# Kernel optimization log

Measured on AMD Instinct MI355X. Metric: run time of the kernel, lower is better.

## Reference

```python
import jax, jax.numpy as jnp
import numpy as np

B, Q, K, D = 16, 2048, 2048, 512


def setup_inputs() -> dict:
    key = jax.random.key(0)
    kq, kk, kv, kl = jax.random.split(key, 4)
    queries = jax.random.normal(kq, (B, Q, D), dtype=jnp.float32)
    keys = jax.random.normal(kk, (B, K, D), dtype=jnp.float32)
    values = jax.random.normal(kv, (B, K, D), dtype=jnp.float32)
    # lengths in [1, K] so no row is fully masked
    valid_lens = jax.random.randint(kl, (B,), 1, K + 1, dtype=jnp.int32)
    return {"queries": queries, "keys": keys, "values": values, "valid_lens": valid_lens}


def reference(queries, keys, values, valid_lens):
    # scores: [B, Q, K]
    scale = 1.0 / jnp.sqrt(jnp.asarray(queries.shape[-1], queries.dtype))
    scores = jnp.einsum('bqd,bkd->bqk', queries, keys) * scale
    # 1D valid_lens: per-batch key-length mask (positions >= len are masked)
    key_pos = jnp.arange(scores.shape[-1])  # [K]
    mask = key_pos[None, None, :] >= valid_lens[:, None, None]  # [B, 1->Q, K]
    scores = jnp.where(mask, -jnp.inf, scores)
    weights = jax.nn.softmax(scores, axis=-1)  # [B, Q, K]
    # dropout is identity in eval mode (deterministic reference)
    context = jnp.einsum('bqk,bkd->bqd', weights, values)  # [B, Q, D]
    return context, weights
```

## Files before the change

### kernel.cpp

```cpp
#include <hip/hip_runtime.h>
#include <stdint.h>

typedef __bf16 bf16_t;
typedef bf16_t bf16x8 __attribute__((ext_vector_type(8)));
typedef bf16_t bf16x4_t __attribute__((ext_vector_type(4)));
typedef float f32x4 __attribute__((ext_vector_type(4)));

#define NB 16
#define NQ 2048
#define NK 2048
#define ND 512
#define SCALE 0.04419417382415922f

typedef __attribute__((address_space(3))) uint32_t lds_u32;
typedef __attribute__((address_space(1))) const uint32_t glb_u32;

__device__ __forceinline__ float4 ld4(const float* p) { return *(const float4*)p; }

__device__ __forceinline__ f32x4 mfma16(bf16x8 a, bf16x8 b, f32x4 c) {
  return __builtin_amdgcn_mfma_f32_16x16x32_bf16(a, b, c, 0, 0, 0);
}

__global__ __launch_bounds__(256) void prep_kernel(const float* __restrict__ Qf,
                                                   const float* __restrict__ Kf,
                                                   const float* __restrict__ Vf,
                                                   bf16_t* __restrict__ Qb,
                                                   bf16_t* __restrict__ Kb,
                                                   bf16_t* __restrict__ VT,
                                                   const int* __restrict__ lens) {
  int x = blockIdx.x;
  int b = blockIdx.y;
  int z = blockIdx.z;
  int t = threadIdx.x;

  if (z == 2) {
    int kb = x >> 2, dq = (x & 3) * 128;
    if (kb * 32 >= lens[b]) return;
    const float* vsrc = Vf + ((size_t)b * NK + kb * 32) * ND;
    bf16_t* dst = VT + ((size_t)(b * 64 + kb)) * (512 * 32);
    __shared__ alignas(16) bf16_t Ls[32][128];
#pragma unroll
    for (int i = 0; i < 4; ++i) {
      int p = i * 256 + t;
      int k = p >> 5, c4 = p & 31;
      float4 v = ld4(vsrc + (size_t)k * ND + dq + c4 * 4);
      union { bf16_t h[4]; uint2 u; } pk;
      pk.h[0] = (bf16_t)v.x; pk.h[1] = (bf16_t)v.y;
      pk.h[2] = (bf16_t)v.z; pk.h[3] = (bf16_t)v.w;
      *(uint2*)(&Ls[k][c4 * 4]) = pk.u;
    }
    __syncthreads();
    int d = dq + (t >> 1);
    int h = t & 1;
    int sr = d >> 1;
#pragma unroll
    for (int gg = 0; gg < 2; ++gg) {
      int g = h * 2 + gg;
      bf16x8 v;
#pragma unroll
      for (int j = 0; j < 8; ++j) v[j] = Ls[g * 8 + j][d - dq];
      int slot = (((d & 1) << 2) | g) ^ (sr & 7);
      *(bf16x8*)(dst + ((size_t)sr * 8 + slot) * 8) = v;
    }
    return;
  }

  const float* src = z ? Kf : Qf;
  bf16_t* dst = z ? Kb : Qb;
  int rt = x >> 4, kt = x & 15;
  const float* s = src + ((size_t)b * 2048 + (size_t)rt * 128) * 512 + kt * 32;
  bf16_t* dtile = dst + (((size_t)b * 16 + rt) * 16 + kt) * 4096;
#pragma unroll
  for (int i = 0; i < 2; ++i) {
    int d = i * 256 + t;
    int r = d >> 2, slot = d & 3;
    int c = slot ^ ((r >> 1) & 3);
    const float* p = s + (size_t)r * 512 + c * 8;
    float4 v0 = ld4(p), v1 = ld4(p + 4);
    bf16x8 o;
    o[0] = (bf16_t)v0.x; o[1] = (bf16_t)v0.y; o[2] = (bf16_t)v0.z; o[3] = (bf16_t)v0.w;
    o[4] = (bf16_t)v1.x; o[5] = (bf16_t)v1.y; o[6] = (bf16_t)v1.z; o[7] = (bf16_t)v1.w;
    *(bf16x8*)(dtile + (size_t)d * 8) = o;
  }
}

__global__ __launch_bounds__(256, 3) void qk_kernel(const bf16_t* __restrict__ Qb,
                                                    const bf16_t* __restrict__ Kb,
                                                    float* __restrict__ P,
                                                    float* __restrict__ psum,
                                                    const int* __restrict__ lens) {
  int bid = blockIdx.x;
  int swz = (bid & 7) * 512 + (bid >> 3);
  int b = swz >> 8;
  int tile = swz & 255;
  int qt = tile >> 4, nt = tile & 15;

  int len = lens[b];
  int q0 = qt * 128;
  int col0 = nt * 128;
  if (col0 >= len) return;

  __shared__ alignas(16) bf16_t As[2][4096];
  __shared__ alignas(16) bf16_t Bs[2][4096];
  __shared__ float rsm[128];

  int t = threadIdx.x;
  int lane = t & 63;
  int wid = t >> 6;
  int wm = wid >> 1, wn = wid & 1;
  int l15 = lane & 15, l4 = lane >> 4;

  float* prow = P + ((size_t)b * NQ + q0) * NK;
  const bf16_t* qtile = Qb + (((size_t)b * 16 + qt) * 16) * 4096;
  const bf16_t* ktile = Kb + (((size_t)b * 16 + nt) * 16) * 4096;

  f32x4 acc[4][4];
  f32x4 zz = {0.f, 0.f, 0.f, 0.f};
#pragma unroll
  for (int mi = 0; mi < 4; ++mi)
#pragma unroll
    for (int ni = 0; ni < 4; ++ni) acc[mi][ni] = zz;

  int eo = wid * 512 + lane * 8;

  auto stage = [&](int kt2, int buf) {
    const bf16_t* qa = qtile + (size_t)kt2 * 4096;
    const bf16_t* ka = ktile + (size_t)kt2 * 4096;
    bf16_t* la = &As[buf][0];
    bf16_t* lb = &Bs[buf][0];
#pragma unroll
    for (int j = 0; j < 2; ++j) {
      __builtin_amdgcn_global_load_lds((glb_u32*)(qa + j * 2048 + eo),
                                       (lds_u32*)(la + j * 2048 + wid * 512), 16, 0, 0);
      __builtin_amdgcn_global_load_lds((glb_u32*)(ka + j * 2048 + eo),
                                       (lds_u32*)(lb + j * 2048 + wid * 512), 16, 0, 0);
    }
  };

  auto compute = [&](int buf) {
    bf16x8 af[4], bv[4];
#pragma unroll
    for (int mi = 0; mi < 4; ++mi) {
      int row = wm * 64 + mi * 16 + l15;
      int ch = row * 4 + (l4 ^ ((row >> 1) & 3));
      af[mi] = *(const bf16x8*)(&As[buf][ch * 8]);
    }
#pragma unroll
    for (int ni = 0; ni < 4; ++ni) {
      int row = wn * 64 + ni * 16 + l15;
      int ch = row * 4 + (l4 ^ ((row >> 1) & 3));
      bv[ni] = *(const bf16x8*)(&Bs[buf][ch * 8]);
    }
#pragma unroll
    for (int mi = 0; mi < 4; ++mi)
#pragma unroll
      for (int ni = 0; ni < 4; ++ni)
        acc[mi][ni] = mfma16(af[mi], bv[ni], acc[mi][ni]);
  };

  stage(0, 0);
  __syncthreads();
#pragma unroll 1
  for (int kt2 = 0; kt2 < 16; ++kt2) {
    if (kt2 + 1 < 16) stage(kt2 + 1, (kt2 + 1) & 1);
    compute(kt2 & 1);
    __syncthreads();
  }

  float rsum[4][4];
#pragma unroll
  for (int mi = 0; mi < 4; ++mi)
#pragma unroll
    for (int r = 0; r < 4; ++r) rsum[mi][r] = 0.f;

#pragma unroll
  for (int mi = 0; mi < 4; ++mi) {
#pragma unroll
    for (int ni = 0; ni < 4; ++ni) {
      int col = col0 + wn * 64 + ni * 16 + l15;
      bool valid = col < len;
#pragma unroll
      for (int r = 0; r < 4; ++r) {
        float e = valid ? __expf(acc[mi][ni][r] * SCALE) : 0.f;
        bf16_t eb = (bf16_t)e;
        rsum[mi][r] += (float)eb;
        bf16_t* purow =
            (bf16_t*)(prow + (size_t)(wm * 64 + mi * 16 + l4 * 4 + r) * NK) + 2048;
        purow[col] = eb;
      }
    }
  }

#pragma unroll
  for (int off = 1; off < 16; off <<= 1)
#pragma unroll
    for (int mi = 0; mi < 4; ++mi)
#pragma unroll
      for (int r = 0; r < 4; ++r)
        rsum[mi][r] += __shfl_xor(rsum[mi][r], off, 64);

  if (wn == 0 && l15 == 0) {
#pragma unroll
    for (int mi = 0; mi < 4; ++mi)
#pragma unroll
      for (int r = 0; r < 4; ++r)
        rsm[wm * 64 + mi * 16 + l4 * 4 + r] = rsum[mi][r];
  }
  __syncthreads();
  if (wn == 1 && l15 == 0) {
#pragma unroll
    for (int mi = 0; mi < 4; ++mi)
#pragma unroll
      for (int r = 0; r < 4; ++r) {
        int row = wm * 64 + mi * 16 + l4 * 4 + r;
        psum[((size_t)b * 16 + nt) * NQ + q0 + row] = rsum[mi][r] + rsm[row];
      }
  }
}

__global__ __launch_bounds__(512, 4) void pv_kernel(float* __restrict__ P,
                                                    const bf16_t* __restrict__ VT,
                                                    float* __restrict__ ctx,
                                                    const float* __restrict__ psum,
                                                    const int* __restrict__ lens) {
  int bid = blockIdx.x;
  int b = bid & 15, qt = bid >> 4;
  int q0 = qt * 64;
  int len = lens[b];
  int nsteps = (len + 31) >> 5;
  int nvalid = (len + 127) >> 7;

  __shared__ alignas(16) bf16_t Ps[2][64 * 32];
  __shared__ float rcp[64];

  int t = threadIdx.x;
  if (t < 64) {
    float s = 0.f;
    for (int i = 0; i < nvalid; ++i) s += psum[((size_t)b * 16 + i) * NQ + q0 + t];
    rcp[t] = 1.0f / s;
  }
  __syncthreads();

  float* prow = P + ((size_t)b * NQ + q0) * NK;
  const bf16_t* vtb = VT + ((size_t)b * 64) * (512 * 32);

  int lane = t & 63, wid = t >> 6;
  int l15 = lane & 15, l4 = lane >> 4;

  f32x4 acc[4][4];
  f32x4 zz = {0.f, 0.f, 0.f, 0.f};
#pragma unroll
  for (int mi = 0; mi < 4; ++mi)
#pragma unroll
    for (int ni = 0; ni < 4; ++ni) acc[mi][ni] = zz;

  int srow = t >> 3, sc4 = t & 7;
  float rr = rcp[srow];
  const bf16_t* purow = (const bf16_t*)(prow + (size_t)srow * NK) + 2048;

  int vchunk[4];
#pragma unroll
  for (int ni = 0; ni < 4; ++ni) {
    int d = wid * 64 + ni * 16 + l15;
    vchunk[ni] = ((d >> 1) * 8 + ((((d & 1) << 2) | l4) ^ ((d >> 1) & 7))) * 8;
  }

  bf16x4_t pld;

  auto stage_load = [&](int ks) {
    pld = *(const bf16x4_t*)(purow + ks * 32 + sc4 * 4);
  };
  auto stage_finish = [&](int ks, int buf) {
    float4 w;
    w.x = (float)pld[0] * rr; w.y = (float)pld[1] * rr;
    w.z = (float)pld[2] * rr; w.w = (float)pld[3] * rr;
    *(float4*)(prow + (size_t)srow * NK + ks * 32 + sc4 * 4) = w;
    int sr = srow >> 1;
    int slot = (((srow & 1) << 2) | (sc4 >> 1)) ^ (sr & 7);
    union { bf16_t h[4]; uint2 u; } pk;
    pk.h[0] = (bf16_t)w.x; pk.h[1] = (bf16_t)w.y;
    pk.h[2] = (bf16_t)w.z; pk.h[3] = (bf16_t)w.w;
    *(uint2*)(&Ps[buf][((size_t)sr * 8 + slot) * 8 + (sc4 & 1) * 4]) = pk.u;
  };
  auto compute = [&](int ks, int cur) {
    const bf16_t* vsrc = vtb + (size_t)ks * (512 * 32);
    bf16x8 bv[4];
#pragma unroll
    for (int ni = 0; ni < 4; ++ni)
      bv[ni] = *(const bf16x8*)(vsrc + vchunk[ni]);
    bf16x8 af[4];
#pragma unroll
    for (int mi = 0; mi < 4; ++mi) {
      int row = mi * 16 + l15;
      af[mi] = *(const bf16x8*)(&Ps[cur][((row >> 1) * 8 + ((((row & 1) << 2) | l4) ^ ((row >> 1) & 7))) * 8]);
    }
#pragma unroll
    for (int mi = 0; mi < 4; ++mi)
#pragma unroll
      for (int ni = 0; ni < 4; ++ni)
        acc[mi][ni] = mfma16(af[mi], bv[ni], acc[mi][ni]);
  };

  stage_load(0);
  stage_finish(0, 0);
  __syncthreads();
#pragma unroll 1
  for (int ks = 0; ks < nsteps; ++ks) {
    int cur = ks & 1;
    if (ks + 1 < nsteps) stage_load(ks + 1);
    compute(ks, cur);
    if (ks + 1 < nsteps) stage_finish(ks + 1, cur ^ 1);
    __syncthreads();
  }

  {
    float4 z = make_float4(0.f, 0.f, 0.f, 0.f);
    for (int c = nsteps * 32 + sc4 * 4; c < NK; c += 32)
      *(float4*)(prow + (size_t)srow * NK + c) = z;
  }

  float* crow = ctx + ((size_t)b * NQ + q0) * ND + wid * 64;
#pragma unroll
  for (int mi = 0; mi < 4; ++mi)
#pragma unroll
    for (int ni = 0; ni < 4; ++ni)
#pragma unroll
      for (int r = 0; r < 4; ++r)
        crow[(size_t)(mi * 16 + l4 * 4 + r) * ND + ni * 16 + l15] = acc[mi][ni][r];
}

extern "C" void kernel_launch(void* const* d_in, const int* in_sizes, int n_in,
                              void* d_out, int out_size, void* d_ws, size_t ws_size,
                              hipStream_t stream) {
  const float* Q = (const float*)d_in[0];
  const float* K = (const float*)d_in[1];
  const float* V = (const float*)d_in[2];
  const int* lens = (const int*)d_in[3];

  float* ctx = (float*)d_out;
  float* P = ctx + (size_t)NB * NQ * ND;

  float* psum = (float*)d_ws;
  char* base = (char*)d_ws + (size_t)NB * 16 * NQ * sizeof(float);
  bf16_t* Qb = (bf16_t*)base;
  bf16_t* Kb = (bf16_t*)(base + (size_t)NB * NQ * ND * 2);
  bf16_t* VT = (bf16_t*)(base + (size_t)2 * NB * NQ * ND * 2);

  prep_kernel<<<dim3(256, 16, 3), 256, 0, stream>>>(Q, K, V, Qb, Kb, VT, lens);
  qk_kernel<<<dim3(4096), 256, 0, stream>>>(Qb, Kb, P, psum, lens);
  pv_kernel<<<dim3(512), 512, 0, stream>>>(P, VT, ctx, psum, lens);
}
```

Before: 284.1 us.

## Enlarge QK tile to 256x256 with 8 waves and deeper k-step

```diff
diff --git a/kernel.cpp b/kernel.cpp
--- a/kernel.cpp
+++ b/kernel.cpp
@@ -84,97 +84,99 @@
   }
 }
 
-__global__ __launch_bounds__(256, 3) void qk_kernel(const bf16_t* __restrict__ Qb,
+__global__ __launch_bounds__(512, 2) void qk_kernel(const bf16_t* __restrict__ Qb,
                                                     const bf16_t* __restrict__ Kb,
                                                     float* __restrict__ P,
                                                     float* __restrict__ psum,
                                                     const int* __restrict__ lens) {
   int bid = blockIdx.x;
-  int swz = (bid & 7) * 512 + (bid >> 3);
-  int b = swz >> 8;
-  int tile = swz & 255;
-  int qt = tile >> 4, nt = tile & 15;
+  int swz = (bid & 7) * 128 + (bid >> 3);
+  int b = swz >> 6;
+  int rest = swz & 63;
+  int qt = rest >> 3, nt = rest & 7;
 
   int len = lens[b];
-  int q0 = qt * 128;
-  int col0 = nt * 128;
+  int q0 = qt * 256;
+  int col0 = nt * 256;
   if (col0 >= len) return;
 
-  __shared__ alignas(16) bf16_t As[2][4096];
-  __shared__ alignas(16) bf16_t Bs[2][4096];
-  __shared__ float rsm[128];
+  __shared__ alignas(16) bf16_t As[2][16384];
+  __shared__ alignas(16) bf16_t Bs[2][16384];
+  float* rsm = (float*)&As[0][0];
 
   int t = threadIdx.x;
   int lane = t & 63;
   int wid = t >> 6;
-  int wm = wid >> 1, wn = wid & 1;
+  int wm = wid >> 2, wn = wid & 3;
   int l15 = lane & 15, l4 = lane >> 4;
 
   float* prow = P + ((size_t)b * NQ + q0) * NK;
-  const bf16_t* qtile = Qb + (((size_t)b * 16 + qt) * 16) * 4096;
-  const bf16_t* ktile = Kb + (((size_t)b * 16 + nt) * 16) * 4096;
-
-  f32x4 acc[4][4];
+  const bf16_t* qbase = Qb + ((size_t)b * 256) * 4096;
+  const bf16_t* kbase = Kb + ((size_t)b * 256) * 4096;
+
+  f32x4 acc[8][4];
   f32x4 zz = {0.f, 0.f, 0.f, 0.f};
 #pragma unroll
-  for (int mi = 0; mi < 4; ++mi)
+  for (int mi = 0; mi < 8; ++mi)
 #pragma unroll
     for (int ni = 0; ni < 4; ++ni) acc[mi][ni] = zz;
 
-  int eo = wid * 512 + lane * 8;
-
-  auto stage = [&](int kt2, int buf) {
-    const bf16_t* qa = qtile + (size_t)kt2 * 4096;
-    const bf16_t* ka = ktile + (size_t)kt2 * 4096;
-    bf16_t* la = &As[buf][0];
-    bf16_t* lb = &Bs[buf][0];
-#pragma unroll
-    for (int j = 0; j < 2; ++j) {
-      __builtin_amdgcn_global_load_lds((glb_u32*)(qa + j * 2048 + eo),
-                                       (lds_u32*)(la + j * 2048 + wid * 512), 16, 0, 0);
-      __builtin_amdgcn_global_load_lds((glb_u32*)(ka + j * 2048 + eo),
-                                       (lds_u32*)(lb + j * 2048 + wid * 512), 16, 0, 0);
+  auto stage = [&](int j, int buf) {
+#pragma unroll
+    for (int u = 0; u < 4; ++u) {
+      int h = u >> 1, s = u & 1;
+      int kt = j * 2 + s;
+      const bf16_t* qa = qbase + ((size_t)((qt * 2 + h) * 16 + kt)) * 4096 + t * 8;
+      const bf16_t* ka = kbase + ((size_t)((nt * 2 + h) * 16 + kt)) * 4096 + t * 8;
+      __builtin_amdgcn_global_load_lds((glb_u32*)qa,
+                                       (lds_u32*)(&As[buf][u * 4096 + wid * 512]), 16, 0, 0);
+      __builtin_amdgcn_global_load_lds((glb_u32*)ka,
+                                       (lds_u32*)(&Bs[buf][u * 4096 + wid * 512]), 16, 0, 0);
     }
   };
 
   auto compute = [&](int buf) {
-    bf16x8 af[4], bv[4];
-#pragma unroll
-    for (int mi = 0; mi < 4; ++mi) {
-      int row = wm * 64 + mi * 16 + l15;
-      int ch = row * 4 + (l4 ^ ((row >> 1) & 3));
-      af[mi] = *(const bf16x8*)(&As[buf][ch * 8]);
-    }
+    bf16x8 bv[4][2];
 #pragma unroll
     for (int ni = 0; ni < 4; ++ni) {
-      int row = wn * 64 + ni * 16 + l15;
-      int ch = row * 4 + (l4 ^ ((row >> 1) & 3));
-      bv[ni] = *(const bf16x8*)(&Bs[buf][ch * 8]);
-    }
-#pragma unroll
-    for (int mi = 0; mi < 4; ++mi)
-#pragma unroll
-      for (int ni = 0; ni < 4; ++ni)
-        acc[mi][ni] = mfma16(af[mi], bv[ni], acc[mi][ni]);
+      int cb = (wn & 1) * 64 + ni * 16 + l15;
+      int hb = wn >> 1;
+      int xr = (cb >> 1) & 3;
+#pragma unroll
+      for (int ks = 0; ks < 2; ++ks)
+        bv[ni][ks] = *(const bf16x8*)(&Bs[buf][(hb * 2 + ks) * 4096 + cb * 32 + (l4 ^ xr) * 8]);
+    }
+#pragma unroll
+    for (int mi = 0; mi < 8; ++mi) {
+      int ra = mi * 16 + l15;
+      int xr = (ra >> 1) & 3;
+      bf16x8 a0 = *(const bf16x8*)(&As[buf][(wm * 2 + 0) * 4096 + ra * 32 + (l4 ^ xr) * 8]);
+      bf16x8 a1 = *(const bf16x8*)(&As[buf][(wm * 2 + 1) * 4096 + ra * 32 + (l4 ^ xr) * 8]);
+#pragma unroll
+      for (int ni = 0; ni < 4; ++ni) {
+        acc[mi][ni] = mfma16(a0, bv[ni][0], acc[mi][ni]);
+        acc[mi][ni] = mfma16(a1, bv[ni][1], acc[mi][ni]);
+      }
+    }
   };
 
   stage(0, 0);
   __syncthreads();
 #pragma unroll 1
-  for (int kt2 = 0; kt2 < 16; ++kt2) {
-    if (kt2 + 1 < 16) stage(kt2 + 1, (kt2 + 1) & 1);
-    compute(kt2 & 1);
+  for (int j = 0; j < 8; ++j) {
+    if (j + 1 < 8) stage(j + 1, (j + 1) & 1);
+    compute(j & 1);
     __syncthreads();
   }
 
-  float rsum[4][4];
-#pragma unroll
-  for (int mi = 0; mi < 4; ++mi)
+  float rsum[8][4];
+#pragma unroll
+  for (int mi = 0; mi < 8; ++mi)
 #pragma unroll
     for (int r = 0; r < 4; ++r) rsum[mi][r] = 0.f;
 
 #pragma unroll
-  for (int mi = 0; mi < 4; ++mi) {
+  for (int mi = 0; mi < 8; ++mi) {
 #pragma unroll
     for (int ni = 0; ni < 4; ++ni) {
       int col = col0 + wn * 64 + ni * 16 + l15;
@@ -185,7 +187,7 @@
         bf16_t eb = (bf16_t)e;
         rsum[mi][r] += (float)eb;
         bf16_t* purow =
-            (bf16_t*)(prow + (size_t)(wm * 64 + mi * 16 + l4 * 4 + r) * NK) + 2048;
+            (bf16_t*)(prow + (size_t)(wm * 128 + mi * 16 + l4 * 4 + r) * NK) + 2048;
         purow[col] = eb;
       }
     }
@@ -194,26 +196,42 @@
 #pragma unroll
   for (int off = 1; off < 16; off <<= 1)
 #pragma unroll
-    for (int mi = 0; mi < 4; ++mi)
+    for (int mi = 0; mi < 8; ++mi)
 #pragma unroll
       for (int r = 0; r < 4; ++r)
         rsum[mi][r] += __shfl_xor(rsum[mi][r], off, 64);
 
   if (wn == 0 && l15 == 0) {
 #pragma unroll
-    for (int mi = 0; mi < 4; ++mi)
-#pragma unroll
-      for (int r = 0; r < 4; ++r)
-        rsm[wm * 64 + mi * 16 + l4 * 4 + r] = rsum[mi][r];
+    for (int mi = 0; mi < 8; ++mi)
+#pragma unroll
+      for (int r = 0; r < 4; ++r)
+        rsm[wm * 128 + mi * 16 + l4 * 4 + r] = rsum[mi][r];
   }
   __syncthreads();
   if (wn == 1 && l15 == 0) {
 #pragma unroll
-    for (int mi = 0; mi < 4; ++mi)
+    for (int mi = 0; mi < 8; ++mi)
+#pragma unroll
+      for (int r = 0; r < 4; ++r)
+        rsm[wm * 128 + mi * 16 + l4 * 4 + r] += rsum[mi][r];
+  }
+  __syncthreads();
+  if (wn == 2 && l15 == 0) {
+#pragma unroll
+    for (int mi = 0; mi < 8; ++mi)
+#pragma unroll
+      for (int r = 0; r < 4; ++r)
+        rsm[wm * 128 + mi * 16 + l4 * 4 + r] += rsum[mi][r];
+  }
+  __syncthreads();
+  if (wn == 3 && l15 == 0) {
+#pragma unroll
+    for (int mi = 0; mi < 8; ++mi)
 #pragma unroll
       for (int r = 0; r < 4; ++r) {
-        int row = wm * 64 + mi * 16 + l4 * 4 + r;
-        psum[((size_t)b * 16 + nt) * NQ + q0 + row] = rsum[mi][r] + rsm[row];
+        int row = wm * 128 + mi * 16 + l4 * 4 + r;
+        psum[((size_t)b * 16 + nt) * NQ + q0 + row] = rsm[row] + rsum[mi][r];
       }
   }
 }
@@ -228,7 +246,7 @@
   int q0 = qt * 64;
   int len = lens[b];
   int nsteps = (len + 31) >> 5;
-  int nvalid = (len + 127) >> 7;
+  int nvalid = (len + 255) >> 8;
 
   __shared__ alignas(16) bf16_t Ps[2][64 * 32];
   __shared__ float rcp[64];
@@ -347,6 +365,6 @@
   bf16_t* VT = (bf16_t*)(base + (size_t)2 * NB * NQ * ND * 2);
 
   prep_kernel<<<dim3(256, 16, 3), 256, 0, stream>>>(Q, K, V, Qb, Kb, VT, lens);
-  qk_kernel<<<dim3(4096), 256, 0, stream>>>(Qb, Kb, P, psum, lens);
+  qk_kernel<<<dim3(1024), 512, 0, stream>>>(Qb, Kb, P, psum, lens);
   pv_kernel<<<dim3(512), 512, 0, stream>>>(P, VT, ctx, psum, lens);
 }
```

Measured after the change: 304.8 us. 1.07x slower.
